# Optimization experiments

Hardware: AMD Instinct MI355X
Metric: run time of the kernel (lower is better)

Reference implementation:

```python
import jax, jax.numpy as jnp
import numpy as np

B, T, D, H, A = 1, 262144, 8, 64, 4  # batch, seq_len, state_dim, hidden, n_actions


def setup_inputs() -> dict:
    key = jax.random.key(0)
    ks = jax.random.split(key, 10)
    s = lambda k, shape, sc: jax.random.normal(k, shape, dtype=jnp.float32) * sc
    return {
        "x": jax.random.normal(ks[0], (B, T, D), dtype=jnp.float32),
        # encoder MLP (Dense->tanh, Dense->tanh)
        "W1": s(ks[1], (D, H), 0.5), "b1": jnp.zeros((H,), jnp.float32),
        "W2": s(ks[2], (H, H), 0.15), "b2": jnp.zeros((H,), jnp.float32),
        # SimpleRNN params: h_t = tanh(x_t @ Wx + h_{t-1} @ Wh + b_rnn)
        "Wx": s(ks[3], (H, H), 0.15), "Wh": s(ks[4], (H, H), 0.1),
        "b_rnn": jnp.zeros((H,), jnp.float32),
        # means head
        "Wm": s(ks[5], (H, A), 0.01), "bm": jnp.zeros((A,), jnp.float32),
    }


def reference(x, W1, b1, W2, b2, Wx, Wh, b_rnn, Wm, bm):
    # Masking(mask_value=0): a timestep is masked if ALL features == 0
    mask = jnp.any(x != 0.0, axis=-1)  # [B, T] bool
    # TimeDistributed encoder (applies pointwise over time -> plain batched matmul)
    h1 = jnp.tanh(x @ W1 + b1)          # [B, T, H]
    h2 = jnp.tanh(h1 @ W2 + b2)         # [B, T, H]
    # Precompute input contribution to the RNN outside the scan (efficient form)
    xz = h2 @ Wx + b_rnn                # [B, T, H]

    def step(h, inp):
        z, m = inp                       # z: [B, H], m: [B]
        h_new = jnp.tanh(z + h @ Wh)
        # masked timesteps: carry previous state through (Keras RNN masking semantics)
        h = jnp.where(m[:, None], h_new, h)
        return h, h

    h0 = jnp.zeros((B, H), x.dtype)
    _, hs = jax.lax.scan(step, h0, (jnp.swapaxes(xz, 0, 1), jnp.swapaxes(mask, 0, 1)))
    hs = jnp.swapaxes(hs, 0, 1)          # [B, T, H]
    means = hs @ Wm + bm                 # [B, T, A]
    return means
```

## Files before the change

### kernel.cpp

```cpp
#include <hip/hip_runtime.h>
#include <hip/hip_bf16.h>

constexpr int T_LEN  = 262144;
constexpr int H      = 64;
constexpr int S_LEN  = 8;
constexpr int WARM   = 16;
constexpr int CHUNKS = T_LEN / S_LEN;
constexpr int NWAVE  = CHUNKS / 16;
constexpr int ZPAD_TAIL = 4;

typedef __attribute__((ext_vector_type(8))) short short8;
typedef __attribute__((ext_vector_type(4))) float f32x4;

__device__ __forceinline__ float fast_tanh(float x) {
    float e = __expf(2.0f * x);
    return 1.0f - 2.0f * __builtin_amdgcn_rcpf(e + 1.0f);
}
__device__ __forceinline__ unsigned short f2bf(float v) {
    unsigned u = __builtin_bit_cast(unsigned, v);
    return (unsigned short)((u + 0x7fffu + ((u >> 16) & 1u)) >> 16);
}
__device__ __forceinline__ float bf2f(unsigned short b) {
    return __builtin_bit_cast(float, (unsigned)b << 16);
}
__device__ __forceinline__ unsigned pack2(float a, float b) {
#if __has_builtin(__builtin_amdgcn_cvt_pk_bf16_f32)
    typedef __attribute__((ext_vector_type(2))) __bf16 bf16x2;
    bf16x2 r = __builtin_amdgcn_cvt_pk_bf16_f32(a, b);
    return __builtin_bit_cast(unsigned, r);
#else
    return (unsigned)f2bf(a) | ((unsigned)f2bf(b) << 16);
#endif
}

__global__ __launch_bounds__(256) void encoder_kernel(
    const float* __restrict__ x,
    const float* __restrict__ W1, const float* __restrict__ b1,
    const float* __restrict__ W2, const float* __restrict__ b2,
    const float* __restrict__ Wx, const float* __restrict__ b_rnn,
    unsigned short* __restrict__ z_s, float* __restrict__ m_s)
{
    __shared__ uint4 w1a[4 * 64];
    __shared__ uint4 w2a[8 * 64];
    __shared__ uint4 w3a[8 * 64];

    const int tid = threadIdx.x;
    const int w   = tid >> 6;
    const int l   = tid & 63;
    const int q   = l >> 4;
    const int n15 = l & 15;

    {
        const int smt = tid >> 6;
        const int sl  = tid & 63;
        const int sq  = sl >> 4;
        const int sn  = sl & 15;
        const int prow = 32 * (smt >> 1) + 8 * (sn >> 2) + 4 * (smt & 1) + (sn & 3);

        uint4 o1 = make_uint4(0, 0, 0, 0);
        if (sq < 2) {
            float v[8];
            #pragma unroll
            for (int j = 0; j < 8; ++j) v[j] = W1[j * 64 + prow];
            o1.x = pack2(v[0], v[1]); o1.y = pack2(v[2], v[3]);
            o1.z = pack2(v[4], v[5]); o1.w = pack2(v[6], v[7]);
        }
        w1a[smt * 64 + sl] = o1;

        #pragma unroll
        for (int kh = 0; kh < 2; ++kh) {
            float v2[8], v3[8];
            #pragma unroll
            for (int j = 0; j < 8; ++j) {
                const int k = kh * 32 + sq * 8 + j;
                v2[j] = W2[k * 64 + prow];
                v3[j] = Wx[k * 64 + prow];
            }
            uint4 o2, o3;
            o2.x = pack2(v2[0], v2[1]); o2.y = pack2(v2[2], v2[3]);
            o2.z = pack2(v2[4], v2[5]); o2.w = pack2(v2[6], v2[7]);
            o3.x = pack2(v3[0], v3[1]); o3.y = pack2(v3[2], v3[3]);
            o3.z = pack2(v3[4], v3[5]); o3.w = pack2(v3[6], v3[7]);
            w2a[(smt * 2 + kh) * 64 + sl] = o2;
            w3a[(smt * 2 + kh) * 64 + sl] = o3;
        }
    }
    __syncthreads();

    f32x4 b1v[4], b2v[4], brv[4];
    #pragma unroll
    for (int mt = 0; mt < 4; ++mt) {
        const int base = 32 * (mt >> 1) + 4 * (mt & 1) + 8 * q;
        b1v[mt] = *(const f32x4*)(b1 + base);
        b2v[mt] = *(const f32x4*)(b2 + base);
        brv[mt] = *(const f32x4*)(b_rnn + base);
    }

    float4 xa, xb;
    {
        const size_t t0 = (size_t)(blockIdx.x * 256 + w * 16 + n15) * 8;
        xa = *(const float4*)(x + t0);
        xb = *(const float4*)(x + t0 + 4);
    }

    #pragma unroll
    for (int it = 0; it < 4; ++it) {
        const int t = blockIdx.x * 256 + it * 64 + w * 16 + n15;

        float4 na = xa, nb = xb;
        if (it < 3) {
            const size_t tn0 = (size_t)(t + 64) * 8;
            na = *(const float4*)(x + tn0);
            nb = *(const float4*)(x + tn0 + 4);
        }

        short8 xB = (short8)0;
        {
            const float xv[8] = {xa.x, xa.y, xa.z, xa.w, xb.x, xb.y, xb.z, xb.w};
            if (q == 0) {
                bool nz = false;
                #pragma unroll
                for (int d = 0; d < 8; ++d) nz = nz || (xv[d] != 0.0f);
                m_s[t] = nz ? 1.0f : 0.0f;
                uint4 o;
                o.x = pack2(xv[0], xv[1]); o.y = pack2(xv[2], xv[3]);
                o.z = pack2(xv[4], xv[5]); o.w = pack2(xv[6], xv[7]);
                xB = __builtin_bit_cast(short8, o);
            } else if (q == 1) {
                float lo[8];
                #pragma unroll
                for (int d = 0; d < 8; ++d) lo[d] = xv[d] - bf2f(f2bf(xv[d]));
                uint4 o;
                o.x = pack2(lo[0], lo[1]); o.y = pack2(lo[2], lo[3]);
                o.z = pack2(lo[4], lo[5]); o.w = pack2(lo[6], lo[7]);
                xB = __builtin_bit_cast(short8, o);
            }
        }

        f32x4 acc[4];
        #pragma unroll
        for (int mt = 0; mt < 4; ++mt)
            acc[mt] = __builtin_amdgcn_mfma_f32_16x16x32_bf16(
                __builtin_bit_cast(short8, w1a[mt * 64 + l]), xB,
                (f32x4){0.f, 0.f, 0.f, 0.f}, 0, 0, 0);

        short8 hb0, hb1;
        {
            unsigned hw[8];
            #pragma unroll
            for (int mt = 0; mt < 4; ++mt) {
                float th[4];
                #pragma unroll
                for (int r = 0; r < 4; ++r)
                    th[r] = fast_tanh(acc[mt][r] + b1v[mt][r]);
                hw[mt * 2 + 0] = pack2(th[0], th[1]);
                hw[mt * 2 + 1] = pack2(th[2], th[3]);
            }
            hb0 = __builtin_bit_cast(short8, make_uint4(hw[0], hw[1], hw[2], hw[3]));
            hb1 = __builtin_bit_cast(short8, make_uint4(hw[4], hw[5], hw[6], hw[7]));
        }

        #pragma unroll
        for (int mt = 0; mt < 4; ++mt) {
            f32x4 d = {0.f, 0.f, 0.f, 0.f};
            d = __builtin_amdgcn_mfma_f32_16x16x32_bf16(
                    __builtin_bit_cast(short8, w2a[(mt * 2 + 0) * 64 + l]), hb0, d, 0, 0, 0);
            d = __builtin_amdgcn_mfma_f32_16x16x32_bf16(
                    __builtin_bit_cast(short8, w2a[(mt * 2 + 1) * 64 + l]), hb1, d, 0, 0, 0);
            acc[mt] = d;
        }
        {
            unsigned hw[8];
            #pragma unroll
            for (int mt = 0; mt < 4; ++mt) {
                float th[4];
                #pragma unroll
                for (int r = 0; r < 4; ++r)
                    th[r] = fast_tanh(acc[mt][r] + b2v[mt][r]);
                hw[mt * 2 + 0] = pack2(th[0], th[1]);
                hw[mt * 2 + 1] = pack2(th[2], th[3]);
            }
            hb0 = __builtin_bit_cast(short8, make_uint4(hw[0], hw[1], hw[2], hw[3]));
            hb1 = __builtin_bit_cast(short8, make_uint4(hw[4], hw[5], hw[6], hw[7]));
        }

        #pragma unroll
        for (int mt = 0; mt < 4; ++mt) {
            f32x4 d = {0.f, 0.f, 0.f, 0.f};
            d = __builtin_amdgcn_mfma_f32_16x16x32_bf16(
                    __builtin_bit_cast(short8, w3a[(mt * 2 + 0) * 64 + l]), hb0, d, 0, 0, 0);
            d = __builtin_amdgcn_mfma_f32_16x16x32_bf16(
                    __builtin_bit_cast(short8, w3a[(mt * 2 + 1) * 64 + l]), hb1, d, 0, 0, 0);
            acc[mt] = d;
        }

        {
            unsigned zw[8];
            #pragma unroll
            for (int mt = 0; mt < 4; ++mt) {
                float z0 = acc[mt][0] + brv[mt][0];
                float z1 = acc[mt][1] + brv[mt][1];
                float z2 = acc[mt][2] + brv[mt][2];
                float z3 = acc[mt][3] + brv[mt][3];
                zw[mt * 2 + 0] = pack2(z0, z1);
                zw[mt * 2 + 1] = pack2(z2, z3);
            }
            unsigned short* dst = z_s + (size_t)t * 64 + 8 * q;
            *(uint4*)(dst)      = make_uint4(zw[0], zw[1], zw[2], zw[3]);
            *(uint4*)(dst + 32) = make_uint4(zw[4], zw[5], zw[6], zw[7]);
        }

        xa = na; xb = nb;
    }
}

__global__ __launch_bounds__(256) void rnn_kernel(
    const unsigned short* __restrict__ z_pad, const float* __restrict__ m_pad,
    const float* __restrict__ Wh, const float* __restrict__ Wm,
    const float* __restrict__ bm, float* __restrict__ out)
{
    const int tid = threadIdx.x;
    const int w   = tid >> 6;
    const int l   = tid & 63;
    const int q   = l >> 4;
    const int n15 = l & 15;
    const int rw  = blockIdx.x * 4 + w;
    const int c   = rw * 16 + n15;

    short8 afrag[8];
    #pragma unroll
    for (int tn = 0; tn < 4; ++tn) {
        const int prow = 32 * (tn >> 1) + 8 * (n15 >> 2) + 4 * (tn & 1) + (n15 & 3);
        #pragma unroll
        for (int kh = 0; kh < 2; ++kh) {
            short8 s;
            #pragma unroll
            for (int j = 0; j < 8; ++j)
                s[j] = (short)f2bf(Wh[(kh * 32 + q * 8 + j) * 64 + prow]);
            afrag[tn * 2 + kh] = s;
        }
    }
    short8 wmf[2];
    #pragma unroll
    for (int kh = 0; kh < 2; ++kh) {
        short8 s;
        #pragma unroll
        for (int j = 0; j < 8; ++j)
            s[j] = (n15 < 4) ? (short)f2bf(Wm[(kh * 32 + q * 8 + j) * 4 + n15]) : (short)0;
        wmf[kh] = s;
    }
    const float4 bmv = *(const float4*)bm;

    short8 hB[2];
    hB[0] = (short8)0;
    hB[1] = (short8)0;

    const unsigned short* zrow = z_pad + (size_t)c * S_LEN * 64;
    const float*          mrow = m_pad + (size_t)c * S_LEN;
    const int tneg = -(c * S_LEN);

    const int zo0 = 8 * q;
    const int zo1 = 8 * q + 4;
    const int zo2 = 8 * q + 32;
    const int zo3 = 8 * q + 36;

    uint2 zb0[4], zb1[4];
    float mb0, mb1;
    {
        zb0[0] = *(const uint2*)(zrow + zo0);
        zb0[1] = *(const uint2*)(zrow + zo1);
        zb0[2] = *(const uint2*)(zrow + zo2);
        zb0[3] = *(const uint2*)(zrow + zo3);
        zb1[0] = *(const uint2*)(zrow + 64 + zo0);
        zb1[1] = *(const uint2*)(zrow + 64 + zo1);
        zb1[2] = *(const uint2*)(zrow + 64 + zo2);
        zb1[3] = *(const uint2*)(zrow + 64 + zo3);
    }
    mb0 = mrow[0];
    mb1 = mrow[1];
    zrow += 128; mrow += 2;

    auto body = [&](uint2* zbuf, float& mref,
                    const unsigned short* zrl, const float* mrl,
                    int stv, bool means_prev, bool may_reset) {
        if (may_reset && rw == 0) {
            if (stv == tneg) {
                hB[0] = (short8)0; hB[1] = (short8)0;
            }
        }
        f32x4 acc[4];
        #pragma unroll
        for (int mt = 0; mt < 4; ++mt) {
            f32x4 d = {0.f, 0.f, 0.f, 0.f};
            d = __builtin_amdgcn_mfma_f32_16x16x32_bf16(afrag[mt * 2 + 0], hB[0], d, 0, 0, 0);
            d = __builtin_amdgcn_mfma_f32_16x16x32_bf16(afrag[mt * 2 + 1], hB[1], d, 0, 0, 0);
            acc[mt] = d;
        }
        if (means_prev) {
            f32x4 a2 = {0.f, 0.f, 0.f, 0.f};
            a2 = __builtin_amdgcn_mfma_f32_16x16x32_bf16(wmf[0], hB[0], a2, 0, 0, 0);
            a2 = __builtin_amdgcn_mfma_f32_16x16x32_bf16(wmf[1], hB[1], a2, 0, 0, 0);
            if (q == 0) {
                const size_t tp = (size_t)c * S_LEN + (stv - 1);
                *(float4*)(out + tp * 4) =
                    make_float4(a2[0] + bmv.x, a2[1] + bmv.y, a2[2] + bmv.z, a2[3] + bmv.w);
            }
        }
        const bool upd = (mref != 0.0f);
        #pragma unroll
        for (int tn = 0; tn < 4; ++tn) {
            const unsigned short* zp = (const unsigned short*)&zbuf[tn];
            float th[4];
            #pragma unroll
            for (int r = 0; r < 4; ++r)
                th[r] = fast_tanh(acc[tn][r] + bf2f(zp[r]));
            const unsigned w0 = pack2(th[0], th[1]);
            const unsigned w1 = pack2(th[2], th[3]);
            unsigned* hw = (unsigned*)&hB[tn >> 1];
            const int wi = (tn & 1) * 2;
            hw[wi + 0] = upd ? w0 : hw[wi + 0];
            hw[wi + 1] = upd ? w1 : hw[wi + 1];
        }
        zbuf[0] = *(const uint2*)(zrl + zo0);
        zbuf[1] = *(const uint2*)(zrl + zo1);
        zbuf[2] = *(const uint2*)(zrl + zo2);
        zbuf[3] = *(const uint2*)(zrl + zo3);
        mref = mrl[0];
    };

    for (int i = 0; i < WARM / 2; ++i) {
        const int st = -WARM + 2 * i;
        body(zb0, mb0, zrow,      mrow,     st,     false, true);
        body(zb1, mb1, zrow + 64, mrow + 1, st + 1, false, true);
        zrow += 128; mrow += 2;
    }

    #pragma unroll
    for (int st = 0; st < S_LEN; ++st) {
        if ((st & 1) == 0)
            body(zb0, mb0, zrow + st * 64, mrow + st, st, st >= 1, st == 0);
        else
            body(zb1, mb1, zrow + st * 64, mrow + st, st, true, false);
    }

    {
        f32x4 a2 = {0.f, 0.f, 0.f, 0.f};
        a2 = __builtin_amdgcn_mfma_f32_16x16x32_bf16(wmf[0], hB[0], a2, 0, 0, 0);
        a2 = __builtin_amdgcn_mfma_f32_16x16x32_bf16(wmf[1], hB[1], a2, 0, 0, 0);
        if (q == 0) {
            const size_t tp = (size_t)c * S_LEN + (S_LEN - 1);
            *(float4*)(out + tp * 4) =
                make_float4(a2[0] + bmv.x, a2[1] + bmv.y, a2[2] + bmv.z, a2[3] + bmv.w);
        }
    }
}

extern "C" void kernel_launch(void* const* d_in, const int* in_sizes, int n_in,
                              void* d_out, int out_size, void* d_ws, size_t ws_size,
                              hipStream_t stream) {
    const float* x     = (const float*)d_in[0];
    const float* W1    = (const float*)d_in[1];
    const float* b1    = (const float*)d_in[2];
    const float* W2    = (const float*)d_in[3];
    const float* b2    = (const float*)d_in[4];
    const float* Wx    = (const float*)d_in[5];
    const float* Wh    = (const float*)d_in[6];
    const float* b_rnn = (const float*)d_in[7];
    const float* Wm    = (const float*)d_in[8];
    const float* bm    = (const float*)d_in[9];
    float* out = (float*)d_out;

    unsigned short* z_pad = (unsigned short*)d_ws;
    const size_t z_rows   = (size_t)(WARM + T_LEN + ZPAD_TAIL);
    float*          m_pad = (float*)((char*)d_ws + z_rows * H * 2);

    unsigned short* z_s = z_pad + (size_t)WARM * H;
    float*          m_s = m_pad + WARM;

    encoder_kernel<<<T_LEN / 256, 256, 0, stream>>>(x, W1, b1, W2, b2, Wx, b_rnn, z_s, m_s);
    rnn_kernel<<<NWAVE / 4, 256, 0, stream>>>(z_pad, m_pad, Wh, Wm, bm, out);
}
```

Before: 128.7 us.

## Fuse encoder and RNN kernels via per-wave LDS staging of z and mask

Merges the encoder and the chunked RNN scan into one kernel. Each wave encodes its own 128 timesteps plus the warm-up window into padded LDS rows instead of writing z and the mask to global workspace, then runs the recurrence reading from LDS. Encoder weights are kept in registers rather than shared memory. This removes one launch and the global round trip for z. In exchange, warm-up timesteps are encoded twice, register pressure rises, and the encode phase is no longer spread across as many blocks.

```diff
diff --git a/kernel.cpp b/kernel.cpp
--- a/kernel.cpp
+++ b/kernel.cpp
@@ -7,7 +7,8 @@
 constexpr int WARM   = 16;
 constexpr int CHUNKS = T_LEN / S_LEN;
 constexpr int NWAVE  = CHUNKS / 16;
-constexpr int ZPAD_TAIL = 4;
+constexpr int ROWS   = WARM + 128;
+constexpr int ZROW_DW = 33;
 
 typedef __attribute__((ext_vector_type(8))) short short8;
 typedef __attribute__((ext_vector_type(4))) float f32x4;
@@ -33,46 +34,44 @@
 #endif
 }
 
-__global__ __launch_bounds__(256) void encoder_kernel(
+__global__ __launch_bounds__(256) void fused_kernel(
     const float* __restrict__ x,
     const float* __restrict__ W1, const float* __restrict__ b1,
     const float* __restrict__ W2, const float* __restrict__ b2,
     const float* __restrict__ Wx, const float* __restrict__ b_rnn,
-    unsigned short* __restrict__ z_s, float* __restrict__ m_s)
+    const float* __restrict__ Wh, const float* __restrict__ Wm,
+    const float* __restrict__ bm, float* __restrict__ out)
 {
-    __shared__ uint4 w1a[4 * 64];
-    __shared__ uint4 w2a[8 * 64];
-    __shared__ uint4 w3a[8 * 64];
+    __shared__ unsigned zsh[4][ROWS * ZROW_DW];
 
     const int tid = threadIdx.x;
     const int w   = tid >> 6;
     const int l   = tid & 63;
     const int q   = l >> 4;
     const int n15 = l & 15;
-
-    {
-        const int smt = tid >> 6;
-        const int sl  = tid & 63;
-        const int sq  = sl >> 4;
-        const int sn  = sl & 15;
-        const int prow = 32 * (smt >> 1) + 8 * (sn >> 2) + 4 * (smt & 1) + (sn & 3);
-
+    const int rw  = blockIdx.x * 4 + w;
+
+    unsigned* zdw = zsh[w];
+
+    short8 w1r[4], w2r[8], w3r[8];
+    #pragma unroll
+    for (int mt = 0; mt < 4; ++mt) {
+        const int prow = 32 * (mt >> 1) + 8 * (n15 >> 2) + 4 * (mt & 1) + (n15 & 3);
         uint4 o1 = make_uint4(0, 0, 0, 0);
-        if (sq < 2) {
+        if (q < 2) {
             float v[8];
             #pragma unroll
             for (int j = 0; j < 8; ++j) v[j] = W1[j * 64 + prow];
             o1.x = pack2(v[0], v[1]); o1.y = pack2(v[2], v[3]);
             o1.z = pack2(v[4], v[5]); o1.w = pack2(v[6], v[7]);
         }
-        w1a[smt * 64 + sl] = o1;
-
+        w1r[mt] = __builtin_bit_cast(short8, o1);
         #pragma unroll
         for (int kh = 0; kh < 2; ++kh) {
             float v2[8], v3[8];
             #pragma unroll
             for (int j = 0; j < 8; ++j) {
-                const int k = kh * 32 + sq * 8 + j;
+                const int k = kh * 32 + q * 8 + j;
                 v2[j] = W2[k * 64 + prow];
                 v3[j] = Wx[k * 64 + prow];
             }
@@ -81,12 +80,10 @@
             o2.z = pack2(v2[4], v2[5]); o2.w = pack2(v2[6], v2[7]);
             o3.x = pack2(v3[0], v3[1]); o3.y = pack2(v3[2], v3[3]);
             o3.z = pack2(v3[4], v3[5]); o3.w = pack2(v3[6], v3[7]);
-            w2a[(smt * 2 + kh) * 64 + sl] = o2;
-            w3a[(smt * 2 + kh) * 64 + sl] = o3;
-        }
-    }
-    __syncthreads();
-
+            w2r[mt * 2 + kh] = __builtin_bit_cast(short8, o2);
+            w3r[mt * 2 + kh] = __builtin_bit_cast(short8, o3);
+        }
+    }
     f32x4 b1v[4], b2v[4], brv[4];
     #pragma unroll
     for (int mt = 0; mt < 4; ++mt) {
@@ -96,22 +93,22 @@
         brv[mt] = *(const f32x4*)(b_rnn + base);
     }
 
-    float4 xa, xb;
-    {
-        const size_t t0 = (size_t)(blockIdx.x * 256 + w * 16 + n15) * 8;
-        xa = *(const float4*)(x + t0);
-        xb = *(const float4*)(x + t0 + 4);
-    }
-
-    #pragma unroll
-    for (int it = 0; it < 4; ++it) {
-        const int t = blockIdx.x * 256 + it * 64 + w * 16 + n15;
+    const int t0_abs = rw * 128 - WARM;
+    auto xoff = [&](int g) {
+        int t = t0_abs + g * 16 + n15;
+        if (t < 0) t = 0;
+        return (size_t)t * 8;
+    };
+    float4 xa = *(const float4*)(x + xoff(0));
+    float4 xb = *(const float4*)(x + xoff(0) + 4);
+
+    for (int g = 0; g < 9; ++g) {
+        const int T = g * 16 + n15;
 
         float4 na = xa, nb = xb;
-        if (it < 3) {
-            const size_t tn0 = (size_t)(t + 64) * 8;
-            na = *(const float4*)(x + tn0);
-            nb = *(const float4*)(x + tn0 + 4);
+        if (g < 8) {
+            na = *(const float4*)(x + xoff(g + 1));
+            nb = *(const float4*)(x + xoff(g + 1) + 4);
         }
 
         short8 xB = (short8)0;
@@ -121,7 +118,7 @@
                 bool nz = false;
                 #pragma unroll
                 for (int d = 0; d < 8; ++d) nz = nz || (xv[d] != 0.0f);
-                m_s[t] = nz ? 1.0f : 0.0f;
+                zdw[T * ZROW_DW + 32] = __builtin_bit_cast(unsigned, nz ? 1.0f : 0.0f);
                 uint4 o;
                 o.x = pack2(xv[0], xv[1]); o.y = pack2(xv[2], xv[3]);
                 o.z = pack2(xv[4], xv[5]); o.w = pack2(xv[6], xv[7]);
@@ -141,8 +138,7 @@
         #pragma unroll
         for (int mt = 0; mt < 4; ++mt)
             acc[mt] = __builtin_amdgcn_mfma_f32_16x16x32_bf16(
-                __builtin_bit_cast(short8, w1a[mt * 64 + l]), xB,
-                (f32x4){0.f, 0.f, 0.f, 0.f}, 0, 0, 0);
+                w1r[mt], xB, (f32x4){0.f, 0.f, 0.f, 0.f}, 0, 0, 0);
 
         short8 hb0, hb1;
         {
@@ -163,10 +159,8 @@
         #pragma unroll
         for (int mt = 0; mt < 4; ++mt) {
             f32x4 d = {0.f, 0.f, 0.f, 0.f};
-            d = __builtin_amdgcn_mfma_f32_16x16x32_bf16(
-                    __builtin_bit_cast(short8, w2a[(mt * 2 + 0) * 64 + l]), hb0, d, 0, 0, 0);
-            d = __builtin_amdgcn_mfma_f32_16x16x32_bf16(
-                    __builtin_bit_cast(short8, w2a[(mt * 2 + 1) * 64 + l]), hb1, d, 0, 0, 0);
+            d = __builtin_amdgcn_mfma_f32_16x16x32_bf16(w2r[mt * 2 + 0], hb0, d, 0, 0, 0);
+            d = __builtin_amdgcn_mfma_f32_16x16x32_bf16(w2r[mt * 2 + 1], hb1, d, 0, 0, 0);
             acc[mt] = d;
         }
         {
@@ -187,45 +181,27 @@
         #pragma unroll
         for (int mt = 0; mt < 4; ++mt) {
             f32x4 d = {0.f, 0.f, 0.f, 0.f};
-            d = __builtin_amdgcn_mfma_f32_16x16x32_bf16(
-                    __builtin_bit_cast(short8, w3a[(mt * 2 + 0) * 64 + l]), hb0, d, 0, 0, 0);
-            d = __builtin_amdgcn_mfma_f32_16x16x32_bf16(
-                    __builtin_bit_cast(short8, w3a[(mt * 2 + 1) * 64 + l]), hb1, d, 0, 0, 0);
+            d = __builtin_amdgcn_mfma_f32_16x16x32_bf16(w3r[mt * 2 + 0], hb0, d, 0, 0, 0);
+            d = __builtin_amdgcn_mfma_f32_16x16x32_bf16(w3r[mt * 2 + 1], hb1, d, 0, 0, 0);
             acc[mt] = d;
         }
-
         {
             unsigned zw[8];
             #pragma unroll
             for (int mt = 0; mt < 4; ++mt) {
-                float z0 = acc[mt][0] + brv[mt][0];
-                float z1 = acc[mt][1] + brv[mt][1];
-                float z2 = acc[mt][2] + brv[mt][2];
-                float z3 = acc[mt][3] + brv[mt][3];
-                zw[mt * 2 + 0] = pack2(z0, z1);
-                zw[mt * 2 + 1] = pack2(z2, z3);
-            }
-            unsigned short* dst = z_s + (size_t)t * 64 + 8 * q;
-            *(uint4*)(dst)      = make_uint4(zw[0], zw[1], zw[2], zw[3]);
-            *(uint4*)(dst + 32) = make_uint4(zw[4], zw[5], zw[6], zw[7]);
+                zw[mt * 2 + 0] = pack2(acc[mt][0] + brv[mt][0], acc[mt][1] + brv[mt][1]);
+                zw[mt * 2 + 1] = pack2(acc[mt][2] + brv[mt][2], acc[mt][3] + brv[mt][3]);
+            }
+            #pragma unroll
+            for (int i = 0; i < 4; ++i) {
+                zdw[T * ZROW_DW + 4 * q + i]      = zw[i];
+                zdw[T * ZROW_DW + 16 + 4 * q + i] = zw[4 + i];
+            }
         }
 
         xa = na; xb = nb;
     }
-}
-
-__global__ __launch_bounds__(256) void rnn_kernel(
-    const unsigned short* __restrict__ z_pad, const float* __restrict__ m_pad,
-    const float* __restrict__ Wh, const float* __restrict__ Wm,
-    const float* __restrict__ bm, float* __restrict__ out)
-{
-    const int tid = threadIdx.x;
-    const int w   = tid >> 6;
-    const int l   = tid & 63;
-    const int q   = l >> 4;
-    const int n15 = l & 15;
-    const int rw  = blockIdx.x * 4 + w;
-    const int c   = rw * 16 + n15;
+    __builtin_amdgcn_wave_barrier();
 
     short8 afrag[8];
     #pragma unroll
@@ -254,39 +230,21 @@
     short8 hB[2];
     hB[0] = (short8)0;
     hB[1] = (short8)0;
-
-    const unsigned short* zrow = z_pad + (size_t)c * S_LEN * 64;
-    const float*          mrow = m_pad + (size_t)c * S_LEN;
+    const int c    = rw * 16 + n15;
     const int tneg = -(c * S_LEN);
 
-    const int zo0 = 8 * q;
-    const int zo1 = 8 * q + 4;
-    const int zo2 = 8 * q + 32;
-    const int zo3 = 8 * q + 36;
-
-    uint2 zb0[4], zb1[4];
-    float mb0, mb1;
-    {
-        zb0[0] = *(const uint2*)(zrow + zo0);
-        zb0[1] = *(const uint2*)(zrow + zo1);
-        zb0[2] = *(const uint2*)(zrow + zo2);
-        zb0[3] = *(const uint2*)(zrow + zo3);
-        zb1[0] = *(const uint2*)(zrow + 64 + zo0);
-        zb1[1] = *(const uint2*)(zrow + 64 + zo1);
-        zb1[2] = *(const uint2*)(zrow + 64 + zo2);
-        zb1[3] = *(const uint2*)(zrow + 64 + zo3);
-    }
-    mb0 = mrow[0];
-    mb1 = mrow[1];
-    zrow += 128; mrow += 2;
-
-    auto body = [&](uint2* zbuf, float& mref,
-                    const unsigned short* zrl, const float* mrl,
-                    int stv, bool means_prev, bool may_reset) {
+    auto body = [&](int st, bool means_prev, bool may_reset) {
+        const unsigned* zd = zdw + (unsigned)(8 * n15 + st + WARM) * ZROW_DW;
+        unsigned zc[8];
+        #pragma unroll
+        for (int i = 0; i < 4; ++i) {
+            zc[i]     = zd[4 * q + i];
+            zc[4 + i] = zd[16 + 4 * q + i];
+        }
+        const float mf = __builtin_bit_cast(float, zd[32]);
+
         if (may_reset && rw == 0) {
-            if (stv == tneg) {
-                hB[0] = (short8)0; hB[1] = (short8)0;
-            }
+            if (st == tneg) { hB[0] = (short8)0; hB[1] = (short8)0; }
         }
         f32x4 acc[4];
         #pragma unroll
@@ -301,15 +259,15 @@
             a2 = __builtin_amdgcn_mfma_f32_16x16x32_bf16(wmf[0], hB[0], a2, 0, 0, 0);
             a2 = __builtin_amdgcn_mfma_f32_16x16x32_bf16(wmf[1], hB[1], a2, 0, 0, 0);
             if (q == 0) {
-                const size_t tp = (size_t)c * S_LEN + (stv - 1);
+                const size_t tp = (size_t)c * S_LEN + (st - 1);
                 *(float4*)(out + tp * 4) =
                     make_float4(a2[0] + bmv.x, a2[1] + bmv.y, a2[2] + bmv.z, a2[3] + bmv.w);
             }
         }
-        const bool upd = (mref != 0.0f);
+        const bool upd = (mf != 0.0f);
         #pragma unroll
         for (int tn = 0; tn < 4; ++tn) {
-            const unsigned short* zp = (const unsigned short*)&zbuf[tn];
+            const unsigned short* zp = (const unsigned short*)&zc[tn * 2];
             float th[4];
             #pragma unroll
             for (int r = 0; r < 4; ++r)
@@ -321,28 +279,11 @@
             hw[wi + 0] = upd ? w0 : hw[wi + 0];
             hw[wi + 1] = upd ? w1 : hw[wi + 1];
         }
-        zbuf[0] = *(const uint2*)(zrl + zo0);
-        zbuf[1] = *(const uint2*)(zrl + zo1);
-        zbuf[2] = *(const uint2*)(zrl + zo2);
-        zbuf[3] = *(const uint2*)(zrl + zo3);
-        mref = mrl[0];
     };
 
-    for (int i = 0; i < WARM / 2; ++i) {
-        const int st = -WARM + 2 * i;
-        body(zb0, mb0, zrow,      mrow,     st,     false, true);
-        body(zb1, mb1, zrow + 64, mrow + 1, st + 1, false, true);
-        zrow += 128; mrow += 2;
-    }
-
-    #pragma unroll
-    for (int st = 0; st < S_LEN; ++st) {
-        if ((st & 1) == 0)
-            body(zb0, mb0, zrow + st * 64, mrow + st, st, st >= 1, st == 0);
-        else
-            body(zb1, mb1, zrow + st * 64, mrow + st, st, true, false);
-    }
-
+    for (int st = -WARM; st < 0; ++st) body(st, false, true);
+    #pragma unroll
+    for (int st = 0; st < S_LEN; ++st) body(st, st >= 1, st == 0);
     {
         f32x4 a2 = {0.f, 0.f, 0.f, 0.f};
         a2 = __builtin_amdgcn_mfma_f32_16x16x32_bf16(wmf[0], hB[0], a2, 0, 0, 0);
@@ -370,13 +311,8 @@
     const float* bm    = (const float*)d_in[9];
     float* out = (float*)d_out;
 
-    unsigned short* z_pad = (unsigned short*)d_ws;
-    const size_t z_rows   = (size_t)(WARM + T_LEN + ZPAD_TAIL);
-    float*          m_pad = (float*)((char*)d_ws + z_rows * H * 2);
-
-    unsigned short* z_s = z_pad + (size_t)WARM * H;
-    float*          m_s = m_pad + WARM;
-
-    encoder_kernel<<<T_LEN / 256, 256, 0, stream>>>(x, W1, b1, W2, b2, Wx, b_rnn, z_s, m_s);
-    rnn_kernel<<<NWAVE / 4, 256, 0, stream>>>(z_pad, m_pad, Wh, Wm, bm, out);
-}
+    (void)d_ws; (void)ws_size;
+
+    fused_kernel<<<NWAVE / 4, 256, 0, stream>>>(
+        x, W1, b1, W2, b2, Wx, b_rnn, Wh, Wm, bm, out);
+}
```

Result: slower. 138.7 us (+7.8%).

## Stage per-wave z and mask rows in swizzled LDS before the recurrence

Applied to the files above, without the earlier changes.

Each wave now bulk-loads its contiguous block of padded z rows (warm-up plus chunk rows) and mask values into shared memory with coalesced 16-byte loads and an XOR swizzle. The recurrence steps then read z and mask from LDS instead of issuing small strided global loads that had to be double-buffered in registers. This takes global latency off the serial dependency chain and simplifies the loop, at the cost of about 23 KB of LDS per wave and an up-front load phase that may reduce occupancy.

```diff
diff --git a/kernel.cpp b/kernel.cpp
--- a/kernel.cpp
+++ b/kernel.cpp
@@ -8,6 +8,9 @@
 constexpr int CHUNKS = T_LEN / S_LEN;
 constexpr int NWAVE  = CHUNKS / 16;
 constexpr int ZPAD_TAIL = 4;
+constexpr int ROWS   = WARM + 128;
+constexpr int ZDW_W  = ROWS * 32;
+constexpr int MROWS  = 192;
 
 typedef __attribute__((ext_vector_type(8))) short short8;
 typedef __attribute__((ext_vector_type(4))) float f32x4;
@@ -219,6 +222,9 @@
     const float* __restrict__ Wh, const float* __restrict__ Wm,
     const float* __restrict__ bm, float* __restrict__ out)
 {
+    __shared__ unsigned zsh[4][ZDW_W];
+    __shared__ float    msh[4][MROWS];
+
     const int tid = threadIdx.x;
     const int w   = tid >> 6;
     const int l   = tid & 63;
@@ -227,6 +233,26 @@
     const int rw  = blockIdx.x * 4 + w;
     const int c   = rw * 16 + n15;
 
+    unsigned* zw_ = zsh[w];
+
+    {
+        const uint4* gz = (const uint4*)(z_pad + (size_t)rw * 128 * 64);
+        #pragma unroll
+        for (int k = 0; k < 18; ++k) {
+            const uint4 v = gz[k * 64 + l];
+            const int row = k * 8 + (l >> 3);
+            const int grp = (l & 7) ^ ((k ^ (l >> 3)) & 7);
+            *(uint4*)(zw_ + row * 32 + grp * 4) = v;
+        }
+        const float* gm = m_pad + (size_t)rw * 128;
+        msh[w][l]       = gm[l];
+        msh[w][64 + l]  = gm[64 + l];
+        msh[w][128 + l] = gm[128 + l];
+    }
+    __builtin_amdgcn_wave_barrier();
+    asm volatile("s_waitcnt lgkmcnt(0)" ::: "memory");
+    __builtin_amdgcn_sched_barrier(0);
+
     short8 afrag[8];
     #pragma unroll
     for (int tn = 0; tn < 4; ++tn) {
@@ -254,39 +280,20 @@
     short8 hB[2];
     hB[0] = (short8)0;
     hB[1] = (short8)0;
-
-    const unsigned short* zrow = z_pad + (size_t)c * S_LEN * 64;
-    const float*          mrow = m_pad + (size_t)c * S_LEN;
     const int tneg = -(c * S_LEN);
 
-    const int zo0 = 8 * q;
-    const int zo1 = 8 * q + 4;
-    const int zo2 = 8 * q + 32;
-    const int zo3 = 8 * q + 36;
-
-    uint2 zb0[4], zb1[4];
-    float mb0, mb1;
-    {
-        zb0[0] = *(const uint2*)(zrow + zo0);
-        zb0[1] = *(const uint2*)(zrow + zo1);
-        zb0[2] = *(const uint2*)(zrow + zo2);
-        zb0[3] = *(const uint2*)(zrow + zo3);
-        zb1[0] = *(const uint2*)(zrow + 64 + zo0);
-        zb1[1] = *(const uint2*)(zrow + 64 + zo1);
-        zb1[2] = *(const uint2*)(zrow + 64 + zo2);
-        zb1[3] = *(const uint2*)(zrow + 64 + zo3);
-    }
-    mb0 = mrow[0];
-    mb1 = mrow[1];
-    zrow += 128; mrow += 2;
-
-    auto body = [&](uint2* zbuf, float& mref,
-                    const unsigned short* zrl, const float* mrl,
-                    int stv, bool means_prev, bool may_reset) {
+    auto body = [&](int st, bool means_prev, bool may_reset) {
+        const int row = 8 * n15 + st + WARM;
+        const int v   = ((row >> 3) ^ row) & 7;
+        const unsigned* zr = zw_ + row * 32;
+        const int g1 = (4 * q) ^ (v << 2);
+        const uint4 z1 = *(const uint4*)(zr + g1);
+        const uint4 z2 = *(const uint4*)(zr + (g1 ^ 16));
+        const unsigned zc[8] = {z1.x, z1.y, z1.z, z1.w, z2.x, z2.y, z2.z, z2.w};
+        const float mf = msh[w][row];
+
         if (may_reset && rw == 0) {
-            if (stv == tneg) {
-                hB[0] = (short8)0; hB[1] = (short8)0;
-            }
+            if (st == tneg) { hB[0] = (short8)0; hB[1] = (short8)0; }
         }
         f32x4 acc[4];
         #pragma unroll
@@ -301,15 +308,15 @@
             a2 = __builtin_amdgcn_mfma_f32_16x16x32_bf16(wmf[0], hB[0], a2, 0, 0, 0);
             a2 = __builtin_amdgcn_mfma_f32_16x16x32_bf16(wmf[1], hB[1], a2, 0, 0, 0);
             if (q == 0) {
-                const size_t tp = (size_t)c * S_LEN + (stv - 1);
+                const size_t tp = (size_t)c * S_LEN + (st - 1);
                 *(float4*)(out + tp * 4) =
                     make_float4(a2[0] + bmv.x, a2[1] + bmv.y, a2[2] + bmv.z, a2[3] + bmv.w);
             }
         }
-        const bool upd = (mref != 0.0f);
+        const bool upd = (mf != 0.0f);
         #pragma unroll
         for (int tn = 0; tn < 4; ++tn) {
-            const unsigned short* zp = (const unsigned short*)&zbuf[tn];
+            const unsigned short* zp = (const unsigned short*)&zc[tn * 2];
             float th[4];
             #pragma unroll
             for (int r = 0; r < 4; ++r)
@@ -321,28 +328,11 @@
             hw[wi + 0] = upd ? w0 : hw[wi + 0];
             hw[wi + 1] = upd ? w1 : hw[wi + 1];
         }
-        zbuf[0] = *(const uint2*)(zrl + zo0);
-        zbuf[1] = *(const uint2*)(zrl + zo1);
-        zbuf[2] = *(const uint2*)(zrl + zo2);
-        zbuf[3] = *(const uint2*)(zrl + zo3);
-        mref = mrl[0];
     };
 
-    for (int i = 0; i < WARM / 2; ++i) {
-        const int st = -WARM + 2 * i;
-        body(zb0, mb0, zrow,      mrow,     st,     false, true);
-        body(zb1, mb1, zrow + 64, mrow + 1, st + 1, false, true);
-        zrow += 128; mrow += 2;
-    }
-
-    #pragma unroll
-    for (int st = 0; st < S_LEN; ++st) {
-        if ((st & 1) == 0)
-            body(zb0, mb0, zrow + st * 64, mrow + st, st, st >= 1, st == 0);
-        else
-            body(zb1, mb1, zrow + st * 64, mrow + st, st, true, false);
-    }
-
+    for (int st = -WARM; st < 0; ++st) body(st, false, true);
+    #pragma unroll
+    for (int st = 0; st < S_LEN; ++st) body(st, st >= 1, st == 0);
     {
         f32x4 a2 = {0.f, 0.f, 0.f, 0.f};
         a2 = __builtin_amdgcn_mfma_f32_16x16x32_bf16(wmf[0], hB[0], a2, 0, 0, 0);
```

Measured after the change: 132.0 us. 2.6% more time.
